# Optimization experiments

Measured on AMD Instinct MI355X. Metric: run time of the kernel, lower is better.

The kernel has to match this reference:

```python
import jax, jax.numpy as jnp
import numpy as np

TWO_PI = 2.0 * np.pi


def setup_inputs() -> dict:
    key = jax.random.key(0)
    ks = jax.random.split(key, 6)
    n1 = n2 = n3 = 20
    nk, ni, nspin = 4, 16, 2
    # Invertible, physically plausible lattice (~8 Bohr cubic cell + jitter)
    A = jnp.eye(3, dtype=jnp.float32) * 8.0 + 0.05 * jax.random.normal(ks[0], (3, 3), jnp.float32)
    k_grid = 0.1 * jax.random.normal(ks[1], (nk, 3), jnp.float32)
    cg_real = jax.random.normal(ks[2], (nspin, nk, ni, n1, n2, n3), jnp.float32)
    cg_imag = jax.random.normal(ks[3], (nspin, nk, ni, n1, n2, n3), jnp.float32)
    # Real-space evaluation grid: fractional coords in [0,1)^3 mapped through A
    frac = jax.random.uniform(ks[4], (n1, n2, n3, 3), jnp.float32)
    r = frac @ A
    return {"A": A, "k_grid": k_grid, "cg_real": cg_real, "cg_imag": cg_imag, "r": r}


def reference(A, k_grid, cg_real, cg_imag, r):
    # cg: [spin, nk, ni, n1, n2, n3] complex plane-wave coefficients
    cg = cg_real + 1j * cg_imag
    n1, n2, n3 = cg.shape[-3:]
    # Integer FFT frequency mesh m -> reciprocal-lattice vectors G = m @ B,
    # B rows are reciprocal basis: B = 2*pi * inv(A)^T  (A rows = lattice vecs)
    f1 = jnp.fft.fftfreq(n1) * n1
    f2 = jnp.fft.fftfreq(n2) * n2
    f3 = jnp.fft.fftfreq(n3) * n3
    m = jnp.stack(jnp.meshgrid(f1, f2, f3, indexing="ij"), axis=-1).astype(A.dtype)  # [n1,n2,n3,3]
    B = TWO_PI * jnp.linalg.inv(A).T
    G = (m @ B).reshape(-1, 3)                      # [nG, 3]
    vol = jnp.abs(jnp.linalg.det(A))
    Rf = r.reshape(-1, 3)                           # [nR, 3]
    # Plane-wave synthesis: psi_{s,k,i}(r) = exp(i k.r)/sqrt(vol) * sum_G c_G exp(i G.r)
    # (equivalent to the triple-nested vmap over the grid dims, fully vectorized)
    phase_g = jnp.exp(1j * (Rf @ G.T))              # [nR, nG] complex
    dens = cg.reshape(*cg.shape[:3], -1)            # [spin, nk, ni, nG]
    psi = jnp.einsum("skin,rn->skir", dens, phase_g)  # [spin, nk, ni, nR]
    phase_k = jnp.exp(1j * (Rf @ k_grid.T))         # [nR, nk]
    psi = psi * jnp.moveaxis(phase_k, 0, -1)[None, :, None, :]
    psi = psi / jnp.sqrt(vol).astype(psi.real.dtype)
    # [spin, nk, ni, n1, n2, n3] -- matches moveaxis(range(3), range(-3,0))
    return psi.reshape(*cg.shape[:3], *r.shape[:-1])
```

## Files before the change

kernel.cpp:

```cpp
#include <hip/hip_runtime.h>

typedef __attribute__((ext_vector_type(4))) float f32x4;
typedef __attribute__((ext_vector_type(8))) short s16x8;

#define NSKIN 128
#define NG    8000
#define NRPT  8000
#define MT    128
#define NT    128
#define KK    32
#define KCH   1000
#define NKC   8
#define NRB   64
#define TPB   512
#define PIT   40

__device__ __forceinline__ float sin_rev(float u){ float r; asm("v_sin_f32 %0, %1" : "=v"(r) : "v"(u)); return r; }
__device__ __forceinline__ float cos_rev(float u){ float r; asm("v_cos_f32 %0, %1" : "=v"(r) : "v"(u)); return r; }
__device__ __forceinline__ unsigned int cvt_pk(float lo, float hi){
    unsigned int r; asm("v_cvt_pk_bf16_f32 %0, %1, %2" : "=v"(r) : "v"(lo), "v"(hi)); return r;
}
__device__ __forceinline__ s16x8 bneg(s16x8 v){
    int4 u = *(int4*)&v;
    u.x ^= 0x80008000; u.y ^= 0x80008000; u.z ^= 0x80008000; u.w ^= 0x80008000;
    return *(s16x8*)&u;
}

__global__ __launch_bounds__(TPB, 4) void bloch_mfma3(
    const float* __restrict__ Amat, const float* __restrict__ kgrid,
    const float* __restrict__ cgr,  const float* __restrict__ cgi,
    const float* __restrict__ rpts, float* __restrict__ out, int out_size)
{
    __shared__ float fracS[NT][4];
    __shared__ float rkS[NT][4];
    __shared__ unsigned int T3[NT][20];
    __shared__ unsigned short Ar[MT][PIT], Ai[MT][PIT];
    __shared__ unsigned short Bc[NT][PIT], Bs[NT][PIT];
    __shared__ float invAS[9];
    __shared__ float scaleS;

    const int tid = threadIdx.x;
    const int bid = blockIdx.x;
    const int kc  = bid & 7;
    const int rb  = bid >> 3;
    const int r_base  = rb * NT;
    const int k_begin = kc * KCH;
    const int k_end   = k_begin + KCH;

    if (tid == 0) {
        float a00=Amat[0],a01=Amat[1],a02=Amat[2];
        float a10=Amat[3],a11=Amat[4],a12=Amat[5];
        float a20=Amat[6],a21=Amat[7],a22=Amat[8];
        float c00 =  (a11*a22 - a12*a21);
        float c01 = -(a10*a22 - a12*a20);
        float c02 =  (a10*a21 - a11*a20);
        float det = a00*c00 + a01*c01 + a02*c02;
        float id  = 1.0f/det;
        invAS[0] =  c00*id;
        invAS[1] = -(a01*a22 - a02*a21)*id;
        invAS[2] =  (a01*a12 - a02*a11)*id;
        invAS[3] =  c01*id;
        invAS[4] =  (a00*a22 - a02*a20)*id;
        invAS[5] = -(a00*a12 - a02*a10)*id;
        invAS[6] =  c02*id;
        invAS[7] = -(a00*a21 - a01*a20)*id;
        invAS[8] =  (a00*a11 - a01*a10)*id;
        scaleS   = rsqrtf(fabsf(det));
    }
    __syncthreads();

    if (tid < NT) {
        int rg = r_base + tid; if (rg > NRPT-1) rg = NRPT-1;
        float r0 = rpts[rg*3+0], r1 = rpts[rg*3+1], r2 = rpts[rg*3+2];
        fracS[tid][0] = r0*invAS[0] + r1*invAS[3] + r2*invAS[6];
        fracS[tid][1] = r0*invAS[1] + r1*invAS[4] + r2*invAS[7];
        fracS[tid][2] = r0*invAS[2] + r1*invAS[5] + r2*invAS[8];
        #pragma unroll
        for (int kk = 0; kk < 4; ++kk)
            rkS[tid][kk] = r0*kgrid[kk*3+0] + r1*kgrid[kk*3+1] + r2*kgrid[kk*3+2];
    }
    __syncthreads();

    for (int e = tid; e < NT*20; e += TPB) {
        int r  = (e * 3277) >> 16;
        int i3 = e - r*20;
        float m3 = (float)(i3 - (i3 >= 10 ? 20 : 0));
        float ang = m3 * fracS[r][2];
        float u = ang - floorf(ang);
        T3[r][i3] = cvt_pk(cos_rev(u), sin_rev(u));
    }

    f32x4 accRe[4][2], accIm[4][2];
    #pragma unroll
    for (int mi = 0; mi < 4; ++mi)
        #pragma unroll
        for (int ni = 0; ni < 2; ++ni) {
            accRe[mi][ni] = (f32x4){0.f,0.f,0.f,0.f};
            accIm[mi][ni] = (f32x4){0.f,0.f,0.f,0.f};
        }

    const int lane = tid & 63;
    const int wid  = tid >> 6;
    const int wm   = wid >> 2;
    const int wn   = wid & 3;
    const int frow = lane & 15;
    const int k0   = (lane >> 4) * 8;

    const int sa      = tid >> 2;
    const int seg     = tid & 3;
    const int rB      = tid >> 2;
    const int quarter = tid & 3;

    const float f0r = fracS[rB][0], f1r = fracS[rB][1];

    float4 pvr0, pvr1, pvi0, pvi1;
    {
        int kg = k_begin + seg*8;
        const float* pr_ = &cgr[(size_t)sa*NG + kg];
        const float* pi_ = &cgi[(size_t)sa*NG + kg];
        pvr0 = *(const float4*)pr_;  pvr1 = *(const float4*)(pr_+4);
        pvi0 = *(const float4*)pi_;  pvi1 = *(const float4*)(pi_+4);
    }

    #pragma unroll 1
    for (int kb = k_begin; kb < k_end; kb += KK) {
        __syncthreads();

        {
            uint4 pr, pi;
            pr.x = cvt_pk(pvr0.x, pvr0.y); pr.y = cvt_pk(pvr0.z, pvr0.w);
            pr.z = cvt_pk(pvr1.x, pvr1.y); pr.w = cvt_pk(pvr1.z, pvr1.w);
            pi.x = cvt_pk(pvi0.x, pvi0.y); pi.y = cvt_pk(pvi0.z, pvi0.w);
            pi.z = cvt_pk(pvi1.x, pvi1.y); pi.w = cvt_pk(pvi1.z, pvi1.w);
            *(uint4*)&Ar[sa][seg*8] = pr;
            *(uint4*)&Ai[sa][seg*8] = pi;
        }
        {
            int g0  = kb + quarter*8;
            int i12 = (g0 * 3277) >> 16;
            int i3_0 = g0 - i12*20;
            int i1a = (i12 * 3277) >> 16; int i2a = i12 - i1a*20;
            int i12b = i12 + 1;
            int i1b = (i12b * 3277) >> 16; int i2b = i12b - i1b*20;
            float m1a = (float)(i1a - (i1a >= 10 ? 20 : 0));
            float m2a = (float)(i2a - (i2a >= 10 ? 20 : 0));
            float m1b = (float)(i1b - (i1b >= 10 ? 20 : 0));
            float m2b = (float)(i2b - (i2b >= 10 ? 20 : 0));
            float aa = m1a*f0r + m2a*f1r; aa -= floorf(aa);
            float ab = m1b*f0r + m2b*f1r; ab -= floorf(ab);
            float ca = cos_rev(aa), sa2 = sin_rev(aa);
            float cb = cos_rev(ab), sb2 = sin_rev(ab);
            float bcv[8], bsv[8];
            #pragma unroll
            for (int j = 0; j < 8; ++j) {
                int t = i3_0 + j;
                bool wr = (t >= 20);
                int i3 = wr ? t - 20 : t;
                unsigned int pk = T3[rB][i3];
                float t3c = __uint_as_float(pk << 16);
                float t3s = __uint_as_float(pk & 0xFFFF0000u);
                float pc = wr ? cb : ca;
                float ps = wr ? sb2 : sa2;
                bcv[j] = pc*t3c - ps*t3s;
                bsv[j] = pc*t3s + ps*t3c;
            }
            uint4 wc, wsn;
            wc.x  = cvt_pk(bcv[0], bcv[1]); wc.y  = cvt_pk(bcv[2], bcv[3]);
            wc.z  = cvt_pk(bcv[4], bcv[5]); wc.w  = cvt_pk(bcv[6], bcv[7]);
            wsn.x = cvt_pk(bsv[0], bsv[1]); wsn.y = cvt_pk(bsv[2], bsv[3]);
            wsn.z = cvt_pk(bsv[4], bsv[5]); wsn.w = cvt_pk(bsv[6], bsv[7]);
            *(uint4*)&Bc[rB][quarter*8] = wc;
            *(uint4*)&Bs[rB][quarter*8] = wsn;
        }
        {
            int kb2 = kb + KK;
            int kg  = kb2 + seg*8;
            if (kb2 < k_end && kg < k_end) {
                const float* pr_ = &cgr[(size_t)sa*NG + kg];
                const float* pi_ = &cgi[(size_t)sa*NG + kg];
                pvr0 = *(const float4*)pr_;  pvr1 = *(const float4*)(pr_+4);
                pvi0 = *(const float4*)pi_;  pvi1 = *(const float4*)(pi_+4);
            } else {
                pvr0 = make_float4(0.f,0.f,0.f,0.f); pvr1 = pvr0;
                pvi0 = pvr0; pvi1 = pvr0;
            }
        }
        __syncthreads();

        s16x8 bcf[2], bsf[2];
        #pragma unroll
        for (int ni = 0; ni < 2; ++ni) {
            int col = wn*32 + ni*16 + frow;
            bcf[ni] = *(const s16x8*)&Bc[col][k0];
            bsf[ni] = *(const s16x8*)&Bs[col][k0];
        }
        #pragma unroll
        for (int mi = 0; mi < 4; ++mi) {
            int row = wm*64 + mi*16 + frow;
            s16x8 arf = *(const s16x8*)&Ar[row][k0];
            s16x8 aif = *(const s16x8*)&Ai[row][k0];
            s16x8 ainf = bneg(aif);
            #pragma unroll
            for (int ni = 0; ni < 2; ++ni) {
                accRe[mi][ni] = __builtin_amdgcn_mfma_f32_16x16x32_bf16(arf,  bcf[ni], accRe[mi][ni], 0, 0, 0);
                accRe[mi][ni] = __builtin_amdgcn_mfma_f32_16x16x32_bf16(ainf, bsf[ni], accRe[mi][ni], 0, 0, 0);
                accIm[mi][ni] = __builtin_amdgcn_mfma_f32_16x16x32_bf16(arf,  bsf[ni], accIm[mi][ni], 0, 0, 0);
                accIm[mi][ni] = __builtin_amdgcn_mfma_f32_16x16x32_bf16(aif,  bcf[ni], accIm[mi][ni], 0, 0, 0);
            }
        }
    }

    const bool write_imag = (out_size >= 2*NSKIN*NRPT);
    const float scale  = scaleS;
    const float inv2pi = 0.15915494309189535f;
    #pragma unroll
    for (int mi = 0; mi < 4; ++mi) {
        const int m0 = wm*64 + mi*16;
        const int kidx = (m0 >> 4) & 3;
        #pragma unroll
        for (int ni = 0; ni < 2; ++ni) {
            int col = wn*32 + ni*16 + frow;
            int rg = r_base + col;
            if (rg < NRPT) {
                float ang = rkS[col][kidx] * inv2pi;
                float u = ang - floorf(ang);
                float ck = cos_rev(u), sk = sin_rev(u);
                #pragma unroll
                for (int v = 0; v < 4; ++v) {
                    int sg = m0 + (lane >> 4)*4 + v;
                    float re = accRe[mi][ni][v];
                    float im = accIm[mi][ni][v];
                    float orr = (re*ck - im*sk) * scale;
                    size_t lin = (size_t)sg * NRPT + rg;
                    if (write_imag) {
                        float oi = (re*sk + im*ck) * scale;
                        size_t idx = lin * 2;
                        if (idx + 1 < (size_t)out_size) {
                            atomicAdd(&out[idx],   orr);
                            atomicAdd(&out[idx+1], oi);
                        }
                    } else {
                        if (lin < (size_t)out_size)
                            atomicAdd(&out[lin], orr);
                    }
                }
            }
        }
    }
}

extern "C" void kernel_launch(void* const* d_in, const int* in_sizes, int n_in,
                              void* d_out, int out_size, void* d_ws, size_t ws_size,
                              hipStream_t stream) {
    const float* Amat  = (const float*)d_in[0];
    const float* kgrid = (const float*)d_in[1];
    const float* cgr   = (const float*)d_in[2];
    const float* cgi   = (const float*)d_in[3];
    const float* rpts  = (const float*)d_in[4];
    float* out = (float*)d_out;

    hipMemsetAsync(d_out, 0, (size_t)out_size * sizeof(float), stream);

    dim3 grid(NRB * NKC);
    bloch_mfma3<<<grid, TPB, 0, stream>>>(Amat, kgrid, cgr, cgi, rpts, out, out_size);
}
```

Measured before the change: 109.7 us.

## Replace T3 phase table with recurrence, swizzle LDS tiles, remap block order

Drops the per-point shared T3 table of exp(i m3 f3) and instead builds the 8 consecutive phase factors by complex rotation from one sin/cos evaluation, with correction factors for the wraparounds at the m3 and i12 boundaries. It also replaces the padded shared arrays with an XOR-swizzled layout to avoid LDS bank conflicts without padding. The sign flip moves from the A fragments to the B fragments, so it is applied 2 times per iteration instead of 4. Block indexing changes so that consecutive blocks share a k-chunk rather than an r-block. The recurrence adds serial multiply dependencies and may accumulate rounding error, which is then cast to bf16.

After: 103.3 us. 5.8% less time.

```diff
diff --git a/kernel.cpp b/kernel.cpp
--- a/kernel.cpp
+++ b/kernel.cpp
@@ -13,7 +13,6 @@
 #define NKC   8
 #define NRB   64
 #define TPB   512
-#define PIT   40
 
 __device__ __forceinline__ float sin_rev(float u){ float r; asm("v_sin_f32 %0, %1" : "=v"(r) : "v"(u)); return r; }
 __device__ __forceinline__ float cos_rev(float u){ float r; asm("v_cos_f32 %0, %1" : "=v"(r) : "v"(u)); return r; }
@@ -25,24 +24,26 @@
     u.x ^= 0x80008000; u.y ^= 0x80008000; u.z ^= 0x80008000; u.w ^= 0x80008000;
     return *(s16x8*)&u;
 }
-
-__global__ __launch_bounds__(TPB, 4) void bloch_mfma3(
+__device__ __forceinline__ int swz(int row, int kg){
+    return row*64 + ((kg ^ ((row>>1)&3))<<4);
+}
+
+__global__ __launch_bounds__(TPB, 4) void bloch_mfma4(
     const float* __restrict__ Amat, const float* __restrict__ kgrid,
     const float* __restrict__ cgr,  const float* __restrict__ cgi,
     const float* __restrict__ rpts, float* __restrict__ out, int out_size)
 {
     __shared__ float fracS[NT][4];
     __shared__ float rkS[NT][4];
-    __shared__ unsigned int T3[NT][20];
-    __shared__ unsigned short Ar[MT][PIT], Ai[MT][PIT];
-    __shared__ unsigned short Bc[NT][PIT], Bs[NT][PIT];
+    __shared__ unsigned short Ar[MT*KK], Ai[MT*KK];
+    __shared__ unsigned short Bc[NT*KK], Bs[NT*KK];
     __shared__ float invAS[9];
     __shared__ float scaleS;
 
     const int tid = threadIdx.x;
     const int bid = blockIdx.x;
-    const int kc  = bid & 7;
-    const int rb  = bid >> 3;
+    const int kc  = bid >> 6;
+    const int rb  = bid & 63;
     const int r_base  = rb * NT;
     const int k_begin = kc * KCH;
     const int k_end   = k_begin + KCH;
@@ -81,15 +82,6 @@
     }
     __syncthreads();
 
-    for (int e = tid; e < NT*20; e += TPB) {
-        int r  = (e * 3277) >> 16;
-        int i3 = e - r*20;
-        float m3 = (float)(i3 - (i3 >= 10 ? 20 : 0));
-        float ang = m3 * fracS[r][2];
-        float u = ang - floorf(ang);
-        T3[r][i3] = cvt_pk(cos_rev(u), sin_rev(u));
-    }
-
     f32x4 accRe[4][2], accIm[4][2];
     #pragma unroll
     for (int mi = 0; mi < 4; ++mi)
@@ -104,14 +96,21 @@
     const int wm   = wid >> 2;
     const int wn   = wid & 3;
     const int frow = lane & 15;
-    const int k0   = (lane >> 4) * 8;
+    const int kq   = lane >> 4;
 
     const int sa      = tid >> 2;
     const int seg     = tid & 3;
-    const int rB      = tid >> 2;
-    const int quarter = tid & 3;
-
-    const float f0r = fracS[rB][0], f1r = fracS[rB][1];
+    const int rB      = sa;
+    const int quarter = seg;
+
+    const float f0r = fracS[rB][0], f1r = fracS[rB][1], f2r = fracS[rB][2];
+
+    float u1 = f2r - floorf(f2r);
+    const float w1c = cos_rev(u1), w1s = sin_rev(u1);
+    float yd = -20.0f * f2r; yd -= floorf(yd);
+    const float wdc = cos_rev(yd), wds = sin_rev(yd);
+    const float w1wdc = w1c*wdc - w1s*wds;
+    const float w1wds = w1c*wds + w1s*wdc;
 
     float4 pvr0, pvr1, pvi0, pvi1;
     {
@@ -132,45 +131,47 @@
             pr.z = cvt_pk(pvr1.x, pvr1.y); pr.w = cvt_pk(pvr1.z, pvr1.w);
             pi.x = cvt_pk(pvi0.x, pvi0.y); pi.y = cvt_pk(pvi0.z, pvi0.w);
             pi.z = cvt_pk(pvi1.x, pvi1.y); pi.w = cvt_pk(pvi1.z, pvi1.w);
-            *(uint4*)&Ar[sa][seg*8] = pr;
-            *(uint4*)&Ai[sa][seg*8] = pi;
+            *(uint4*)((char*)Ar + swz(sa, seg)) = pr;
+            *(uint4*)((char*)Ai + swz(sa, seg)) = pi;
         }
         {
-            int g0  = kb + quarter*8;
-            int i12 = (g0 * 3277) >> 16;
+            int g0   = kb + quarter*8;
+            int i12  = (g0 * 3277) >> 16;
             int i3_0 = g0 - i12*20;
-            int i1a = (i12 * 3277) >> 16; int i2a = i12 - i1a*20;
+            int i1a  = (i12 * 3277) >> 16; int i2a = i12 - i1a*20;
             int i12b = i12 + 1;
-            int i1b = (i12b * 3277) >> 16; int i2b = i12b - i1b*20;
+            int i1b  = (i12b * 3277) >> 16; int i2b = i12b - i1b*20;
             float m1a = (float)(i1a - (i1a >= 10 ? 20 : 0));
             float m2a = (float)(i2a - (i2a >= 10 ? 20 : 0));
             float m1b = (float)(i1b - (i1b >= 10 ? 20 : 0));
             float m2b = (float)(i2b - (i2b >= 10 ? 20 : 0));
-            float aa = m1a*f0r + m2a*f1r; aa -= floorf(aa);
-            float ab = m1b*f0r + m2b*f1r; ab -= floorf(ab);
-            float ca = cos_rev(aa), sa2 = sin_rev(aa);
-            float cb = cos_rev(ab), sb2 = sin_rev(ab);
+            float m30 = (float)(i3_0 - (i3_0 >= 10 ? 20 : 0));
+            float y0 = m1a*f0r + m2a*f1r + m30*f2r; y0 -= floorf(y0);
+            float cc = cos_rev(y0), cs = sin_rev(y0);
+            float rd = (m1b-m1a)*f0r + (m2b-m2a)*f1r; rd -= floorf(rd);
+            float rc = cos_rev(rd), rs = sin_rev(rd);
+            float wXc = w1c*rc - w1s*rs;
+            float wXs = w1c*rs + w1s*rc;
             float bcv[8], bsv[8];
+            bcv[0] = cc; bsv[0] = cs;
             #pragma unroll
-            for (int j = 0; j < 8; ++j) {
-                int t = i3_0 + j;
-                bool wr = (t >= 20);
-                int i3 = wr ? t - 20 : t;
-                unsigned int pk = T3[rB][i3];
-                float t3c = __uint_as_float(pk << 16);
-                float t3s = __uint_as_float(pk & 0xFFFF0000u);
-                float pc = wr ? cb : ca;
-                float ps = wr ? sb2 : sa2;
-                bcv[j] = pc*t3c - ps*t3s;
-                bsv[j] = pc*t3s + ps*t3c;
+            for (int j = 1; j < 8; ++j) {
+                bool cB = (i3_0 == 20 - j);
+                bool cD = (i3_0 == 10 - j);
+                float mc = cB ? wXc : (cD ? w1wdc : w1c);
+                float ms = cB ? wXs : (cD ? w1wds : w1s);
+                float nc = cc*mc - cs*ms;
+                float ns = cc*ms + cs*mc;
+                cc = nc; cs = ns;
+                bcv[j] = cc; bsv[j] = cs;
             }
             uint4 wc, wsn;
             wc.x  = cvt_pk(bcv[0], bcv[1]); wc.y  = cvt_pk(bcv[2], bcv[3]);
             wc.z  = cvt_pk(bcv[4], bcv[5]); wc.w  = cvt_pk(bcv[6], bcv[7]);
             wsn.x = cvt_pk(bsv[0], bsv[1]); wsn.y = cvt_pk(bsv[2], bsv[3]);
             wsn.z = cvt_pk(bsv[4], bsv[5]); wsn.w = cvt_pk(bsv[6], bsv[7]);
-            *(uint4*)&Bc[rB][quarter*8] = wc;
-            *(uint4*)&Bs[rB][quarter*8] = wsn;
+            *(uint4*)((char*)Bc + swz(rB, quarter)) = wc;
+            *(uint4*)((char*)Bs + swz(rB, quarter)) = wsn;
         }
         {
             int kb2 = kb + KK;
@@ -187,25 +188,25 @@
         }
         __syncthreads();
 
-        s16x8 bcf[2], bsf[2];
+        s16x8 bcf[2], bsf[2], bsnf[2];
         #pragma unroll
         for (int ni = 0; ni < 2; ++ni) {
             int col = wn*32 + ni*16 + frow;
-            bcf[ni] = *(const s16x8*)&Bc[col][k0];
-            bsf[ni] = *(const s16x8*)&Bs[col][k0];
+            bcf[ni]  = *(const s16x8*)((const char*)Bc + swz(col, kq));
+            bsf[ni]  = *(const s16x8*)((const char*)Bs + swz(col, kq));
+            bsnf[ni] = bneg(bsf[ni]);
         }
         #pragma unroll
         for (int mi = 0; mi < 4; ++mi) {
             int row = wm*64 + mi*16 + frow;
-            s16x8 arf = *(const s16x8*)&Ar[row][k0];
-            s16x8 aif = *(const s16x8*)&Ai[row][k0];
-            s16x8 ainf = bneg(aif);
+            s16x8 arf = *(const s16x8*)((const char*)Ar + swz(row, kq));
+            s16x8 aif = *(const s16x8*)((const char*)Ai + swz(row, kq));
             #pragma unroll
             for (int ni = 0; ni < 2; ++ni) {
-                accRe[mi][ni] = __builtin_amdgcn_mfma_f32_16x16x32_bf16(arf,  bcf[ni], accRe[mi][ni], 0, 0, 0);
-                accRe[mi][ni] = __builtin_amdgcn_mfma_f32_16x16x32_bf16(ainf, bsf[ni], accRe[mi][ni], 0, 0, 0);
-                accIm[mi][ni] = __builtin_amdgcn_mfma_f32_16x16x32_bf16(arf,  bsf[ni], accIm[mi][ni], 0, 0, 0);
-                accIm[mi][ni] = __builtin_amdgcn_mfma_f32_16x16x32_bf16(aif,  bcf[ni], accIm[mi][ni], 0, 0, 0);
+                accRe[mi][ni] = __builtin_amdgcn_mfma_f32_16x16x32_bf16(arf, bcf[ni],  accRe[mi][ni], 0, 0, 0);
+                accRe[mi][ni] = __builtin_amdgcn_mfma_f32_16x16x32_bf16(aif, bsnf[ni], accRe[mi][ni], 0, 0, 0);
+                accIm[mi][ni] = __builtin_amdgcn_mfma_f32_16x16x32_bf16(arf, bsf[ni],  accIm[mi][ni], 0, 0, 0);
+                accIm[mi][ni] = __builtin_amdgcn_mfma_f32_16x16x32_bf16(aif, bcf[ni],  accIm[mi][ni], 0, 0, 0);
             }
         }
     }
@@ -262,5 +263,5 @@
     hipMemsetAsync(d_out, 0, (size_t)out_size * sizeof(float), stream);
 
     dim3 grid(NRB * NKC);
-    bloch_mfma3<<<grid, TPB, 0, stream>>>(Amat, kgrid, cgr, cgi, rpts, out, out_size);
-}
+    bloch_mfma4<<<grid, TPB, 0, stream>>>(Amat, kgrid, cgr, cgi, rpts, out, out_size);
+}
```
